# Optimization experiments

Hardware: AMD Instinct MI355X
Metric: run time of the kernel (lower is better)

The kernel has to match this reference:

```python
import jax, jax.numpy as jnp
import numpy as np

B, N, D, E, R, K = 4, 2048, 1024, 8, 256, 2


def setup_inputs() -> dict:
    key = jax.random.key(0)
    ks = jax.random.split(key, 5)
    scale = 0.02
    return {
        "x": jax.random.normal(ks[0], (B, N, D), dtype=jnp.float32),
        "gate_w": jax.random.normal(ks[1], (D, E), dtype=jnp.float32) * scale,
        "Wu": jax.random.normal(ks[2], (E, D, R), dtype=jnp.float32) * scale,
        "Wv": jax.random.normal(ks[3], (E, D, R), dtype=jnp.float32) * scale,
        "Wo": jax.random.normal(ks[4], (E, R, D), dtype=jnp.float32) * scale,
    }


def reference(x, gate_w, Wu, Wv, Wo):
    # Router: top-k over expert logits, softmax over the selected k logits.
    logits = jnp.einsum("bnd,de->bne", x, gate_w)          # [B,N,E]
    topv, topi = jax.lax.top_k(logits, K)                    # [B,N,K]
    w = jax.nn.softmax(topv, axis=-1)                        # [B,N,K]

    # Dense all-expert SwiGLU (matches reference semantics: every expert
    # computed for every token, then gathered by top-k index).
    u = jnp.einsum("bnd,edr->bner", x, Wu)                  # [B,N,E,R]
    v = jnp.einsum("bnd,edr->bner", x, Wv)                  # [B,N,E,R]
    s = jax.nn.silu(u) * v                                   # [B,N,E,R]
    Y = jnp.einsum("bner,erd->bned", s, Wo)                 # [B,N,E,D]

    # Gather the k selected experts per token and combine with gate weights.
    y_sel = jnp.take_along_axis(Y, topi[..., None], axis=2)  # [B,N,K,D]
    out = jnp.einsum("bnkd,bnk->bnd", y_sel, w)             # [B,N,D]
    return out
```

## Files before the change

### kernel.cpp

```cpp
#include <hip/hip_runtime.h>
#include <math.h>

#define BN 8192
#define DIM 1024
#define NE 8
#define RR 256

using bf16x8 = __attribute__((ext_vector_type(8))) short;
using f32x4  = __attribute__((ext_vector_type(4))) float;

__device__ inline unsigned short f2bf(float f) {
    unsigned int u = __float_as_uint(f);
    u = (u + 0x7fffu + ((u >> 16) & 1u)) >> 16;
    return (unsigned short)u;
}

__global__ __launch_bounds__(256) void k_gwt(const float* __restrict__ gw,
                                             float* __restrict__ gwT) {
    int i = blockIdx.x * 256 + threadIdx.x;
    float v = gw[i];
    int d = i >> 3, e = i & 7;
    gwT[e * DIM + d] = v;
}

__global__ __launch_bounds__(256) void k_router3(const float* __restrict__ x,
                                                 const float* __restrict__ gwT,
                                                 int* __restrict__ topi,
                                                 float* __restrict__ topw,
                                                 unsigned short* __restrict__ xb) {
    int wid  = (blockIdx.x * blockDim.x + threadIdx.x) >> 6;
    int lane = threadIdx.x & 63;
    const float* xp = x + (size_t)wid * DIM + lane * 4;
    unsigned short* xbp = xb + (size_t)wid * DIM + lane * 4;
    float4 acc[NE];
#pragma unroll
    for (int e = 0; e < NE; ++e) acc[e] = float4{0.f, 0.f, 0.f, 0.f};
#pragma unroll
    for (int k = 0; k < 4; ++k) {
        float4 xv = *(const float4*)(xp + k * 256);
        ushort4 us = { f2bf(xv.x), f2bf(xv.y), f2bf(xv.z), f2bf(xv.w) };
        *(ushort4*)(xbp + k * 256) = us;
#pragma unroll
        for (int e = 0; e < NE; ++e) {
            float4 gv = *(const float4*)(gwT + e * DIM + k * 256 + lane * 4);
            acc[e].x += xv.x * gv.x; acc[e].y += xv.y * gv.y;
            acc[e].z += xv.z * gv.z; acc[e].w += xv.w * gv.w;
        }
    }
    float lg[NE];
#pragma unroll
    for (int e = 0; e < NE; ++e)
        lg[e] = (acc[e].x + acc[e].y) + (acc[e].z + acc[e].w);
#pragma unroll
    for (int off = 32; off; off >>= 1) {
#pragma unroll
        for (int e = 0; e < NE; ++e) lg[e] += __shfl_xor(lg[e], off, 64);
    }
    if (lane == 0) {
        float best = lg[0]; int bi = 0;
#pragma unroll
        for (int e = 1; e < NE; ++e) if (lg[e] > best) { best = lg[e]; bi = e; }
        float sec = -3.4e38f; int si = 0;
#pragma unroll
        for (int e = 0; e < NE; ++e) if (e != bi && lg[e] > sec) { sec = lg[e]; si = e; }
        float p  = __expf(sec - best);
        float w0 = 1.f / (1.f + p);
        float w1 = p * w0;
        topi[wid * 2 + 0] = bi;  topw[wid * 2 + 0] = w0;
        topi[wid * 2 + 1] = si;  topw[wid * 2 + 1] = w1;
    }
}

__global__ __launch_bounds__(1024) void k_count_scan(const int* __restrict__ topi,
                                                     int* __restrict__ counts,
                                                     int* __restrict__ offsets,
                                                     int* __restrict__ fill,
                                                     int* __restrict__ tileOff) {
    __shared__ int sh[1024 * NE];
    int tid = threadIdx.x;
    int c[NE];
#pragma unroll
    for (int j = 0; j < NE; ++j) c[j] = 0;
    const int4* tp = (const int4*)topi;
    for (int i = tid; i < BN * 2 / 4; i += 1024) {
        int4 v = tp[i];
#pragma unroll
        for (int j = 0; j < NE; ++j)
            c[j] += (v.x == j) + (v.y == j) + (v.z == j) + (v.w == j);
    }
#pragma unroll
    for (int j = 0; j < NE; ++j) sh[tid * NE + j] = c[j];
    __syncthreads();
    for (int s = 512; s > 0; s >>= 1) {
        if (tid < s) {
#pragma unroll
            for (int j = 0; j < NE; ++j) sh[tid * NE + j] += sh[(tid + s) * NE + j];
        }
        __syncthreads();
    }
    if (tid == 0) {
        int acc = 0, tacc = 0;
        for (int j = 0; j < NE; ++j) {
            int cj = sh[j];
            counts[j]  = cj;
            offsets[j] = acc;   acc  += cj;
            tileOff[j] = tacc;  tacc += (cj + 63) >> 6;
        }
        tileOff[NE] = tacc;
    }
    if (tid < NE) fill[tid] = 0;
}

__global__ __launch_bounds__(256) void k_fill2(const int* __restrict__ topi,
                                               const float* __restrict__ topw,
                                               const int* __restrict__ offsets,
                                               int* __restrict__ fill,
                                               int* __restrict__ btok,
                                               float* __restrict__ bw,
                                               int* __restrict__ slotOf) {
    int tid = threadIdx.x;
    int i = blockIdx.x * 256 + tid;
    int w = tid >> 6, lane = tid & 63;
    int e = topi[i];
    float wt = topw[i];

    __shared__ int waveCnt[4][NE];
    __shared__ int wavePre[4][NE];
    __shared__ int baseSh[NE];

    int myrank = 0;
    unsigned long long lt = (1ull << lane) - 1ull;
#pragma unroll
    for (int j = 0; j < NE; ++j) {
        unsigned long long m = __ballot(e == j);
        if (e == j) myrank = __popcll(m & lt);
        if (lane == 0) waveCnt[w][j] = __popcll(m);
    }
    __syncthreads();
    if (tid < NE) {
        int j = tid, acc = 0;
#pragma unroll
        for (int ww = 0; ww < 4; ++ww) { wavePre[ww][j] = acc; acc += waveCnt[ww][j]; }
        baseSh[j] = atomicAdd(&fill[j], acc);
    }
    __syncthreads();
    int slot = offsets[e] + baseSh[e] + wavePre[w][e] + myrank;
    btok[slot] = i >> 1;
    bw[slot]   = wt;
    slotOf[i]  = slot;
}

__global__ __launch_bounds__(256) void k_cvt3(const float* __restrict__ Wu,
                                              const float* __restrict__ Wv,
                                              const float* __restrict__ Wo,
                                              unsigned short* __restrict__ Wub,
                                              unsigned short* __restrict__ Wvb,
                                              unsigned short* __restrict__ Wob) {
    int z = blockIdx.y;
    int which = z >> 3, e = z & 7;
    int tile = blockIdx.x;
    const float* in; unsigned short* out;
    int M, N, n0, m0;
    if (which < 2) {
        M = DIM; N = RR;
        n0 = (tile & 7) * 32;  m0 = (tile >> 3) * 32;
        in = which ? Wv : Wu;  out = which ? Wvb : Wub;
    } else {
        M = RR; N = DIM;
        n0 = (tile & 31) * 32; m0 = (tile >> 5) * 32;
        in = Wo; out = Wob;
    }
    __shared__ float t[32][33];
    int tx = threadIdx.x & 31, ty = threadIdx.x >> 5;
    const float* inE = in + (size_t)e * M * N;
    unsigned short* outE = out + (size_t)e * M * N;
#pragma unroll
    for (int i = ty; i < 32; i += 8)
        t[i][tx] = inE[(size_t)(m0 + i) * N + n0 + tx];
    __syncthreads();
#pragma unroll
    for (int i = ty; i < 32; i += 8)
        outE[(size_t)(n0 + i) * M + m0 + tx] = f2bf(t[tx][i]);
}

__global__ __launch_bounds__(256, 2) void k_uv(
        const unsigned short* __restrict__ xb,
        const unsigned short* __restrict__ Wub,
        const unsigned short* __restrict__ Wvb,
        const int* __restrict__ counts,
        const int* __restrict__ offsets,
        const int* __restrict__ tileOff,
        const int* __restrict__ btok,
        const float* __restrict__ bw,
        unsigned short* __restrict__ Sbuf) {
    int rt = blockIdx.x & 3;
    int mt_lin = blockIdx.x >> 2;
    if (mt_lin >= tileOff[NE]) return;
    int e = 0;
#pragma unroll
    for (int j = 1; j < NE; ++j) if (mt_lin >= tileOff[j]) e = j;
    int t0 = (mt_lin - tileOff[e]) * 64;
    int ne = counts[e];
    int nt = min(64, ne - t0);
    int start = offsets[e] + t0;

    int tid = threadIdx.x;
    int w = tid >> 6, lane = tid & 63;
    int m16 = lane & 15, quad = lane >> 4;
    int wm = w & 1, wn = w >> 1;

    __shared__ unsigned short As[64][72];
    __shared__ unsigned short Bs[128][72];
    __shared__ int   tokL[64];
    __shared__ float gwL[64];

    if (tid < 64) {
        tokL[tid] = (tid < nt) ? btok[start + tid] : btok[start];
        gwL[tid]  = (tid < nt) ? bw[start + tid] : 0.f;
    }
    __syncthreads();

    const unsigned short* WuE = Wub + (size_t)e * RR * DIM + (size_t)rt * 64 * DIM;
    const unsigned short* WvE = Wvb + (size_t)e * RR * DIM + (size_t)rt * 64 * DIM;

    int arow = tid >> 2, apart = tid & 3;
    const unsigned short* asrc = xb + (size_t)tokL[arow] * DIM + apart * 16;
    int brow = tid >> 1, bhalf = tid & 1;
    const unsigned short* bsrc =
        (brow < 64 ? WuE + (size_t)brow * DIM : WvE + (size_t)(brow - 64) * DIM)
        + bhalf * 32;

    f32x4 accU[2][2], accV[2][2];
    f32x4 zz = {0.f, 0.f, 0.f, 0.f};
#pragma unroll
    for (int mt = 0; mt < 2; ++mt)
#pragma unroll
        for (int nl = 0; nl < 2; ++nl) { accU[mt][nl] = zz; accV[mt][nl] = zz; }

    uint4 pa0 = *(const uint4*)(asrc);
    uint4 pa1 = *(const uint4*)(asrc + 8);
    uint4 pb0 = *(const uint4*)(bsrc);
    uint4 pb1 = *(const uint4*)(bsrc + 8);
    uint4 pb2 = *(const uint4*)(bsrc + 16);
    uint4 pb3 = *(const uint4*)(bsrc + 24);

    for (int kt = 0; kt < 16; ++kt) {
        __syncthreads();
        *(uint4*)&As[arow][apart * 16]      = pa0;
        *(uint4*)&As[arow][apart * 16 + 8]  = pa1;
        *(uint4*)&Bs[brow][bhalf * 32]      = pb0;
        *(uint4*)&Bs[brow][bhalf * 32 + 8]  = pb1;
        *(uint4*)&Bs[brow][bhalf * 32 + 16] = pb2;
        *(uint4*)&Bs[brow][bhalf * 32 + 24] = pb3;
        __syncthreads();
        if (kt < 15) {
            int k1 = (kt + 1) * 64;
            pa0 = *(const uint4*)(asrc + k1);
            pa1 = *(const uint4*)(asrc + k1 + 8);
            pb0 = *(const uint4*)(bsrc + k1);
            pb1 = *(const uint4*)(bsrc + k1 + 8);
            pb2 = *(const uint4*)(bsrc + k1 + 16);
            pb3 = *(const uint4*)(bsrc + k1 + 24);
        }
#pragma unroll
        for (int ks = 0; ks < 2; ++ks) {
            bf16x8 a[2], bu[2], bv[2];
#pragma unroll
            for (int mt = 0; mt < 2; ++mt)
                a[mt] = *(const bf16x8*)&As[wm * 32 + mt * 16 + m16][ks * 32 + quad * 8];
#pragma unroll
            for (int nl = 0; nl < 2; ++nl) {
                bu[nl] = *(const bf16x8*)&Bs[wn * 32 + nl * 16 + m16][ks * 32 + quad * 8];
                bv[nl] = *(const bf16x8*)&Bs[64 + wn * 32 + nl * 16 + m16][ks * 32 + quad * 8];
            }
#pragma unroll
            for (int nl = 0; nl < 2; ++nl)
#pragma unroll
                for (int mt = 0; mt < 2; ++mt) {
                    accU[mt][nl] = __builtin_amdgcn_mfma_f32_16x16x32_bf16(a[mt], bu[nl], accU[mt][nl], 0, 0, 0);
                    accV[mt][nl] = __builtin_amdgcn_mfma_f32_16x16x32_bf16(a[mt], bv[nl], accV[mt][nl], 0, 0, 0);
                }
        }
    }

#pragma unroll
    for (int mt = 0; mt < 2; ++mt)
#pragma unroll
        for (int nl = 0; nl < 2; ++nl)
#pragma unroll
            for (int reg = 0; reg < 4; ++reg) {
                int trow = wm * 32 + mt * 16 + quad * 4 + reg;
                int rcol = rt * 64 + wn * 32 + nl * 16 + m16;
                float u = accU[mt][nl][reg], v = accV[mt][nl][reg];
                float s = (u / (1.f + __expf(-u))) * v * gwL[trow];
                if (trow < nt)
                    Sbuf[(size_t)(start + trow) * RR + rcol] = f2bf(s);
            }
}

__global__ __launch_bounds__(256, 2) void k_down(
        const unsigned short* __restrict__ Sbuf,
        const unsigned short* __restrict__ Wob,
        const int* __restrict__ counts,
        const int* __restrict__ offsets,
        const int* __restrict__ tileOff,
        const int* __restrict__ btok,
        float* __restrict__ ybuf,
        float* __restrict__ out) {
    int nd = blockIdx.x & 7;
    int mt_lin = blockIdx.x >> 3;
    if (mt_lin >= tileOff[NE]) return;
    int e = 0;
#pragma unroll
    for (int j = 1; j < NE; ++j) if (mt_lin >= tileOff[j]) e = j;
    int t0 = (mt_lin - tileOff[e]) * 64;
    int ne = counts[e];
    int nt = min(64, ne - t0);
    int start = offsets[e] + t0;

    int tid = threadIdx.x;
    int w = tid >> 6, lane = tid & 63;
    int m16 = lane & 15, quad = lane >> 4;
    int wm = w & 1, wn = w >> 1;

    __shared__ unsigned short As[64][72];
    __shared__ unsigned short Bs[128][72];
    __shared__ int tokL[64];

    if (tid < 64)
        tokL[tid] = (tid < nt) ? btok[start + tid] : btok[start];
    __syncthreads();

    const unsigned short* WoE = Wob + (size_t)e * DIM * RR + (size_t)nd * 128 * RR;

    int arow = tid >> 2, apart = tid & 3;
    const unsigned short* asrc = Sbuf + (size_t)(start + arow) * RR + apart * 16;
    int brow = tid >> 1, bhalf = tid & 1;
    const unsigned short* bsrc = WoE + (size_t)brow * RR + bhalf * 32;

    f32x4 acc[2][4];
    f32x4 zz = {0.f, 0.f, 0.f, 0.f};
#pragma unroll
    for (int mt = 0; mt < 2; ++mt)
#pragma unroll
        for (int nl = 0; nl < 4; ++nl) acc[mt][nl] = zz;

    uint4 pa0 = *(const uint4*)(asrc);
    uint4 pa1 = *(const uint4*)(asrc + 8);
    uint4 pb0 = *(const uint4*)(bsrc);
    uint4 pb1 = *(const uint4*)(bsrc + 8);
    uint4 pb2 = *(const uint4*)(bsrc + 16);
    uint4 pb3 = *(const uint4*)(bsrc + 24);

    for (int kt = 0; kt < 4; ++kt) {
        __syncthreads();
        *(uint4*)&As[arow][apart * 16]      = pa0;
        *(uint4*)&As[arow][apart * 16 + 8]  = pa1;
        *(uint4*)&Bs[brow][bhalf * 32]      = pb0;
        *(uint4*)&Bs[brow][bhalf * 32 + 8]  = pb1;
        *(uint4*)&Bs[brow][bhalf * 32 + 16] = pb2;
        *(uint4*)&Bs[brow][bhalf * 32 + 24] = pb3;
        __syncthreads();
        if (kt < 3) {
            int k1 = (kt + 1) * 64;
            pa0 = *(const uint4*)(asrc + k1);
            pa1 = *(const uint4*)(asrc + k1 + 8);
            pb0 = *(const uint4*)(bsrc + k1);
            pb1 = *(const uint4*)(bsrc + k1 + 8);
            pb2 = *(const uint4*)(bsrc + k1 + 16);
            pb3 = *(const uint4*)(bsrc + k1 + 24);
        }
#pragma unroll
        for (int ks = 0; ks < 2; ++ks) {
            bf16x8 a[2], b[4];
#pragma unroll
            for (int mt = 0; mt < 2; ++mt)
                a[mt] = *(const bf16x8*)&As[wm * 32 + mt * 16 + m16][ks * 32 + quad * 8];
#pragma unroll
            for (int nl = 0; nl < 4; ++nl)
                b[nl] = *(const bf16x8*)&Bs[wn * 64 + nl * 16 + m16][ks * 32 + quad * 8];
#pragma unroll
            for (int nl = 0; nl < 4; ++nl)
#pragma unroll
                for (int mt = 0; mt < 2; ++mt)
                    acc[mt][nl] = __builtin_amdgcn_mfma_f32_16x16x32_bf16(a[mt], b[nl], acc[mt][nl], 0, 0, 0);
        }
    }

    if (ybuf) {
#pragma unroll
        for (int mt = 0; mt < 2; ++mt)
#pragma unroll
            for (int nl = 0; nl < 4; ++nl)
#pragma unroll
                for (int reg = 0; reg < 4; ++reg) {
                    int srow = wm * 32 + mt * 16 + quad * 4 + reg;
                    int d    = nd * 128 + wn * 64 + nl * 16 + m16;
                    if (srow < nt)
                        ybuf[(size_t)(start + srow) * DIM + d] = acc[mt][nl][reg];
                }
    } else {
#pragma unroll
        for (int mt = 0; mt < 2; ++mt)
#pragma unroll
            for (int nl = 0; nl < 4; ++nl)
#pragma unroll
                for (int reg = 0; reg < 4; ++reg) {
                    int srow = wm * 32 + mt * 16 + quad * 4 + reg;
                    int d    = nd * 128 + wn * 64 + nl * 16 + m16;
                    if (srow < nt)
                        atomicAdd(&out[(size_t)tokL[srow] * DIM + d], acc[mt][nl][reg]);
                }
    }
}

__global__ __launch_bounds__(256) void k_combine(const float* __restrict__ ybuf,
                                                 const int* __restrict__ slotOf,
                                                 float* __restrict__ out) {
    int t   = blockIdx.x;
    int seg = threadIdx.x;
    int s0 = slotOf[t * 2 + 0];
    int s1 = slotOf[t * 2 + 1];
    float4 a = *(const float4*)(ybuf + (size_t)s0 * DIM + seg * 4);
    float4 b = *(const float4*)(ybuf + (size_t)s1 * DIM + seg * 4);
    float4 r = { a.x + b.x, a.y + b.y, a.z + b.z, a.w + b.w };
    *(float4*)(out + (size_t)t * DIM + seg * 4) = r;
}

extern "C" void kernel_launch(void* const* d_in, const int* in_sizes, int n_in,
                              void* d_out, int out_size, void* d_ws, size_t ws_size,
                              hipStream_t stream) {
    const float* x  = (const float*)d_in[0];
    const float* gw = (const float*)d_in[1];
    const float* Wu = (const float*)d_in[2];
    const float* Wv = (const float*)d_in[3];
    const float* Wo = (const float*)d_in[4];
    float* out = (float*)d_out;

    int*   wsi     = (int*)d_ws;
    int*   counts  = wsi + 0;
    int*   offsets = wsi + 8;
    int*   fill    = wsi + 16;
    int*   tileOff = wsi + 24;
    int*   topi    = wsi + 48;
    float* topw    = (float*)(wsi + 48 + 16384);
    int*   btok    = wsi + 48 + 32768;
    float* bw      = (float*)(wsi + 48 + 49152);
    int*   slotOf  = wsi + 48 + 65536;
    float* gwT     = (float*)((char*)d_ws + 327872);

    const size_t off_xb  = 393216;
    const size_t off_wub = off_xb  + (size_t)BN * DIM * 2;
    const size_t off_wvb = off_wub + (size_t)NE * RR * DIM * 2;
    const size_t off_wob = off_wvb + (size_t)NE * RR * DIM * 2;
    const size_t off_sb  = off_wob + (size_t)NE * DIM * RR * 2;
    const size_t off_yb  = off_sb  + (size_t)(BN * 2 + 128) * RR * 2;
    const size_t need_yb = off_yb  + (size_t)BN * 2 * DIM * 4;

    unsigned short* xb   = (unsigned short*)((char*)d_ws + off_xb);
    unsigned short* Wub  = (unsigned short*)((char*)d_ws + off_wub);
    unsigned short* Wvb  = (unsigned short*)((char*)d_ws + off_wvb);
    unsigned short* Wob  = (unsigned short*)((char*)d_ws + off_wob);
    unsigned short* Sbuf = (unsigned short*)((char*)d_ws + off_sb);
    bool use_ybuf = (ws_size >= need_yb);
    float* ybuf = use_ybuf ? (float*)((char*)d_ws + off_yb) : nullptr;

    k_gwt<<<dim3(DIM * NE / 256), 256, 0, stream>>>(gw, gwT);
    k_router3<<<dim3(BN / 4), 256, 0, stream>>>(x, gwT, topi, topw, xb);
    k_count_scan<<<1, 1024, 0, stream>>>(topi, counts, offsets, fill, tileOff);
    k_fill2<<<dim3(BN * 2 / 256), 256, 0, stream>>>(topi, topw, offsets, fill,
                                                    btok, bw, slotOf);
    k_cvt3<<<dim3(256, 24), 256, 0, stream>>>(Wu, Wv, Wo, Wub, Wvb, Wob);

    if (!use_ybuf)
        hipMemsetAsync(d_out, 0, (size_t)BN * DIM * sizeof(float), stream);

    k_uv<<<dim3(264 * 4), 256, 0, stream>>>(xb, Wub, Wvb, counts, offsets, tileOff,
                                            btok, bw, Sbuf);
    k_down<<<dim3(264 * 8), 256, 0, stream>>>(Sbuf, Wob, counts, offsets, tileOff,
                                              btok, ybuf, out);
    if (use_ybuf)
        k_combine<<<dim3(BN), 256, 0, stream>>>(ybuf, slotOf, out);
}
```

Before: 204.8 us.

## Load expert weights directly into registers and widen per-block tiles in MoE GEMMs

In both the up/gate and down-projection kernels, the B-operand (weights) is now read straight from global memory into MFMA register fragments with a one-step register prefetch, instead of being staged through shared memory. Each wave now covers a full 64-row by 64-column slice, so k_uv covers all 256 R columns per block and k_down covers 256 output columns per block, cutting grid sizes by 4x and 2x. The A tile is double-buffered in LDS, which drops one barrier per k-step. The cost is much higher register pressure from the 32 accumulators in k_uv, which may lower occupancy, and fewer blocks in k_uv (264), which may underfill the GPU.

```diff
diff --git a/kernel.cpp b/kernel.cpp
--- a/kernel.cpp
+++ b/kernel.cpp
@@ -193,8 +193,7 @@
         const int* __restrict__ btok,
         const float* __restrict__ bw,
         unsigned short* __restrict__ Sbuf) {
-    int rt = blockIdx.x & 3;
-    int mt_lin = blockIdx.x >> 2;
+    int mt_lin = blockIdx.x;
     if (mt_lin >= tileOff[NE]) return;
     int e = 0;
 #pragma unroll
@@ -207,10 +206,8 @@
     int tid = threadIdx.x;
     int w = tid >> 6, lane = tid & 63;
     int m16 = lane & 15, quad = lane >> 4;
-    int wm = w & 1, wn = w >> 1;
-
-    __shared__ unsigned short As[64][72];
-    __shared__ unsigned short Bs[128][72];
+
+    __shared__ unsigned short As[2][64][72];
     __shared__ int   tokL[64];
     __shared__ float gwL[64];
 
@@ -220,77 +217,78 @@
     }
     __syncthreads();
 
-    const unsigned short* WuE = Wub + (size_t)e * RR * DIM + (size_t)rt * 64 * DIM;
-    const unsigned short* WvE = Wvb + (size_t)e * RR * DIM + (size_t)rt * 64 * DIM;
+    const unsigned short* WuE = Wub + (size_t)e * RR * DIM;
+    const unsigned short* WvE = Wvb + (size_t)e * RR * DIM;
 
     int arow = tid >> 2, apart = tid & 3;
     const unsigned short* asrc = xb + (size_t)tokL[arow] * DIM + apart * 16;
-    int brow = tid >> 1, bhalf = tid & 1;
-    const unsigned short* bsrc =
-        (brow < 64 ? WuE + (size_t)brow * DIM : WvE + (size_t)(brow - 64) * DIM)
-        + bhalf * 32;
-
-    f32x4 accU[2][2], accV[2][2];
+
+    const unsigned short* buBase = WuE + (size_t)(w * 64 + m16) * DIM + quad * 8;
+    const unsigned short* bvBase = WvE + (size_t)(w * 64 + m16) * DIM + quad * 8;
+
+    f32x4 accU[4][4], accV[4][4];
     f32x4 zz = {0.f, 0.f, 0.f, 0.f};
 #pragma unroll
-    for (int mt = 0; mt < 2; ++mt)
-#pragma unroll
-        for (int nl = 0; nl < 2; ++nl) { accU[mt][nl] = zz; accV[mt][nl] = zz; }
+    for (int mt = 0; mt < 4; ++mt)
+#pragma unroll
+        for (int nl = 0; nl < 4; ++nl) { accU[mt][nl] = zz; accV[mt][nl] = zz; }
 
     uint4 pa0 = *(const uint4*)(asrc);
     uint4 pa1 = *(const uint4*)(asrc + 8);
-    uint4 pb0 = *(const uint4*)(bsrc);
-    uint4 pb1 = *(const uint4*)(bsrc + 8);
-    uint4 pb2 = *(const uint4*)(bsrc + 16);
-    uint4 pb3 = *(const uint4*)(bsrc + 24);
+    uint4 bu[4], bv[4];
+#pragma unroll
+    for (int nl = 0; nl < 4; ++nl) {
+        bu[nl] = *(const uint4*)(buBase + nl * 16 * DIM);
+        bv[nl] = *(const uint4*)(bvBase + nl * 16 * DIM);
+    }
 
     for (int kt = 0; kt < 16; ++kt) {
+        int buf = kt & 1;
+        *(uint4*)&As[buf][arow][apart * 16]     = pa0;
+        *(uint4*)&As[buf][arow][apart * 16 + 8] = pa1;
+        if (kt < 15) {
+            pa0 = *(const uint4*)(asrc + (kt + 1) * 64);
+            pa1 = *(const uint4*)(asrc + (kt + 1) * 64 + 8);
+        }
         __syncthreads();
-        *(uint4*)&As[arow][apart * 16]      = pa0;
-        *(uint4*)&As[arow][apart * 16 + 8]  = pa1;
-        *(uint4*)&Bs[brow][bhalf * 32]      = pb0;
-        *(uint4*)&Bs[brow][bhalf * 32 + 8]  = pb1;
-        *(uint4*)&Bs[brow][bhalf * 32 + 16] = pb2;
-        *(uint4*)&Bs[brow][bhalf * 32 + 24] = pb3;
-        __syncthreads();
-        if (kt < 15) {
-            int k1 = (kt + 1) * 64;
-            pa0 = *(const uint4*)(asrc + k1);
-            pa1 = *(const uint4*)(asrc + k1 + 8);
-            pb0 = *(const uint4*)(bsrc + k1);
-            pb1 = *(const uint4*)(bsrc + k1 + 8);
-            pb2 = *(const uint4*)(bsrc + k1 + 16);
-            pb3 = *(const uint4*)(bsrc + k1 + 24);
-        }
 #pragma unroll
         for (int ks = 0; ks < 2; ++ks) {
-            bf16x8 a[2], bu[2], bv[2];
-#pragma unroll
-            for (int mt = 0; mt < 2; ++mt)
-                a[mt] = *(const bf16x8*)&As[wm * 32 + mt * 16 + m16][ks * 32 + quad * 8];
-#pragma unroll
-            for (int nl = 0; nl < 2; ++nl) {
-                bu[nl] = *(const bf16x8*)&Bs[wn * 32 + nl * 16 + m16][ks * 32 + quad * 8];
-                bv[nl] = *(const bf16x8*)&Bs[64 + wn * 32 + nl * 16 + m16][ks * 32 + quad * 8];
+            uint4 nu[4], nv[4];
+            int kn = kt * 64 + ks * 32 + 32;
+            if (kt < 15 || ks < 1) {
+#pragma unroll
+                for (int nl = 0; nl < 4; ++nl) {
+                    nu[nl] = *(const uint4*)(buBase + nl * 16 * DIM + kn);
+                    nv[nl] = *(const uint4*)(bvBase + nl * 16 * DIM + kn);
+                }
             }
-#pragma unroll
-            for (int nl = 0; nl < 2; ++nl)
-#pragma unroll
-                for (int mt = 0; mt < 2; ++mt) {
-                    accU[mt][nl] = __builtin_amdgcn_mfma_f32_16x16x32_bf16(a[mt], bu[nl], accU[mt][nl], 0, 0, 0);
-                    accV[mt][nl] = __builtin_amdgcn_mfma_f32_16x16x32_bf16(a[mt], bv[nl], accV[mt][nl], 0, 0, 0);
+            bf16x8 a[4];
+#pragma unroll
+            for (int mt = 0; mt < 4; ++mt)
+                a[mt] = *(const bf16x8*)&As[buf][mt * 16 + m16][ks * 32 + quad * 8];
+#pragma unroll
+            for (int nl = 0; nl < 4; ++nl) {
+                bf16x8 fu = __builtin_bit_cast(bf16x8, bu[nl]);
+                bf16x8 fv = __builtin_bit_cast(bf16x8, bv[nl]);
+#pragma unroll
+                for (int mt = 0; mt < 4; ++mt) {
+                    accU[mt][nl] = __builtin_amdgcn_mfma_f32_16x16x32_bf16(a[mt], fu, accU[mt][nl], 0, 0, 0);
+                    accV[mt][nl] = __builtin_amdgcn_mfma_f32_16x16x32_bf16(a[mt], fv, accV[mt][nl], 0, 0, 0);
                 }
-        }
-    }
-
-#pragma unroll
-    for (int mt = 0; mt < 2; ++mt)
-#pragma unroll
-        for (int nl = 0; nl < 2; ++nl)
+            }
+#pragma unroll
+            for (int nl = 0; nl < 4; ++nl) { bu[nl] = nu[nl]; bv[nl] = nv[nl]; }
+        }
+    }
+
+#pragma unroll
+    for (int mt = 0; mt < 4; ++mt)
+#pragma unroll
+        for (int nl = 0; nl < 4; ++nl)
 #pragma unroll
             for (int reg = 0; reg < 4; ++reg) {
-                int trow = wm * 32 + mt * 16 + quad * 4 + reg;
-                int rcol = rt * 64 + wn * 32 + nl * 16 + m16;
+                int trow = mt * 16 + quad * 4 + reg;
+                int rcol = w * 64 + nl * 16 + m16;
                 float u = accU[mt][nl][reg], v = accV[mt][nl][reg];
                 float s = (u / (1.f + __expf(-u))) * v * gwL[trow];
                 if (trow < nt)
@@ -307,8 +305,8 @@
         const int* __restrict__ btok,
         float* __restrict__ ybuf,
         float* __restrict__ out) {
-    int nd = blockIdx.x & 7;
-    int mt_lin = blockIdx.x >> 3;
+    int nd = blockIdx.x & 3;
+    int mt_lin = blockIdx.x >> 2;
     if (mt_lin >= tileOff[NE]) return;
     int e = 0;
 #pragma unroll
@@ -321,93 +319,90 @@
     int tid = threadIdx.x;
     int w = tid >> 6, lane = tid & 63;
     int m16 = lane & 15, quad = lane >> 4;
-    int wm = w & 1, wn = w >> 1;
-
-    __shared__ unsigned short As[64][72];
-    __shared__ unsigned short Bs[128][72];
+
+    __shared__ unsigned short As[2][64][72];
     __shared__ int tokL[64];
 
     if (tid < 64)
         tokL[tid] = (tid < nt) ? btok[start + tid] : btok[start];
     __syncthreads();
 
-    const unsigned short* WoE = Wob + (size_t)e * DIM * RR + (size_t)nd * 128 * RR;
+    const unsigned short* WoE = Wob + (size_t)e * DIM * RR;
 
     int arow = tid >> 2, apart = tid & 3;
     const unsigned short* asrc = Sbuf + (size_t)(start + arow) * RR + apart * 16;
-    int brow = tid >> 1, bhalf = tid & 1;
-    const unsigned short* bsrc = WoE + (size_t)brow * RR + bhalf * 32;
-
-    f32x4 acc[2][4];
+
+    const unsigned short* bBase = WoE + (size_t)(nd * 256 + w * 64 + m16) * RR + quad * 8;
+
+    f32x4 acc[4][4];
     f32x4 zz = {0.f, 0.f, 0.f, 0.f};
 #pragma unroll
-    for (int mt = 0; mt < 2; ++mt)
+    for (int mt = 0; mt < 4; ++mt)
 #pragma unroll
         for (int nl = 0; nl < 4; ++nl) acc[mt][nl] = zz;
 
     uint4 pa0 = *(const uint4*)(asrc);
     uint4 pa1 = *(const uint4*)(asrc + 8);
-    uint4 pb0 = *(const uint4*)(bsrc);
-    uint4 pb1 = *(const uint4*)(bsrc + 8);
-    uint4 pb2 = *(const uint4*)(bsrc + 16);
-    uint4 pb3 = *(const uint4*)(bsrc + 24);
+    uint4 b[4];
+#pragma unroll
+    for (int nl = 0; nl < 4; ++nl)
+        b[nl] = *(const uint4*)(bBase + nl * 16 * RR);
 
     for (int kt = 0; kt < 4; ++kt) {
+        int buf = kt & 1;
+        *(uint4*)&As[buf][arow][apart * 16]     = pa0;
+        *(uint4*)&As[buf][arow][apart * 16 + 8] = pa1;
+        if (kt < 3) {
+            pa0 = *(const uint4*)(asrc + (kt + 1) * 64);
+            pa1 = *(const uint4*)(asrc + (kt + 1) * 64 + 8);
+        }
         __syncthreads();
-        *(uint4*)&As[arow][apart * 16]      = pa0;
-        *(uint4*)&As[arow][apart * 16 + 8]  = pa1;
-        *(uint4*)&Bs[brow][bhalf * 32]      = pb0;
-        *(uint4*)&Bs[brow][bhalf * 32 + 8]  = pb1;
-        *(uint4*)&Bs[brow][bhalf * 32 + 16] = pb2;
-        *(uint4*)&Bs[brow][bhalf * 32 + 24] = pb3;
-        __syncthreads();
-        if (kt < 3) {
-            int k1 = (kt + 1) * 64;
-            pa0 = *(const uint4*)(asrc + k1);
-            pa1 = *(const uint4*)(asrc + k1 + 8);
-            pb0 = *(const uint4*)(bsrc + k1);
-            pb1 = *(const uint4*)(bsrc + k1 + 8);
-            pb2 = *(const uint4*)(bsrc + k1 + 16);
-            pb3 = *(const uint4*)(bsrc + k1 + 24);
-        }
 #pragma unroll
         for (int ks = 0; ks < 2; ++ks) {
-            bf16x8 a[2], b[4];
-#pragma unroll
-            for (int mt = 0; mt < 2; ++mt)
-                a[mt] = *(const bf16x8*)&As[wm * 32 + mt * 16 + m16][ks * 32 + quad * 8];
+            uint4 nb[4];
+            int kn = kt * 64 + ks * 32 + 32;
+            if (kt < 3 || ks < 1) {
+#pragma unroll
+                for (int nl = 0; nl < 4; ++nl)
+                    nb[nl] = *(const uint4*)(bBase + nl * 16 * RR + kn);
+            }
+            bf16x8 a[4];
+#pragma unroll
+            for (int mt = 0; mt < 4; ++mt)
+                a[mt] = *(const bf16x8*)&As[buf][mt * 16 + m16][ks * 32 + quad * 8];
+#pragma unroll
+            for (int nl = 0; nl < 4; ++nl) {
+                bf16x8 fb = __builtin_bit_cast(bf16x8, b[nl]);
+#pragma unroll
+                for (int mt = 0; mt < 4; ++mt)
+                    acc[mt][nl] = __builtin_amdgcn_mfma_f32_16x16x32_bf16(a[mt], fb, acc[mt][nl], 0, 0, 0);
+            }
+#pragma unroll
+            for (int nl = 0; nl < 4; ++nl) b[nl] = nb[nl];
+        }
+    }
+
+    if (ybuf) {
+#pragma unroll
+        for (int mt = 0; mt < 4; ++mt)
 #pragma unroll
             for (int nl = 0; nl < 4; ++nl)
-                b[nl] = *(const bf16x8*)&Bs[wn * 64 + nl * 16 + m16][ks * 32 + quad * 8];
-#pragma unroll
-            for (int nl = 0; nl < 4; ++nl)
-#pragma unroll
-                for (int mt = 0; mt < 2; ++mt)
-                    acc[mt][nl] = __builtin_amdgcn_mfma_f32_16x16x32_bf16(a[mt], b[nl], acc[mt][nl], 0, 0, 0);
-        }
-    }
-
-    if (ybuf) {
-#pragma unroll
-        for (int mt = 0; mt < 2; ++mt)
-#pragma unroll
-            for (int nl = 0; nl < 4; ++nl)
 #pragma unroll
                 for (int reg = 0; reg < 4; ++reg) {
-                    int srow = wm * 32 + mt * 16 + quad * 4 + reg;
-                    int d    = nd * 128 + wn * 64 + nl * 16 + m16;
+                    int srow = mt * 16 + quad * 4 + reg;
+                    int d    = nd * 256 + w * 64 + nl * 16 + m16;
                     if (srow < nt)
                         ybuf[(size_t)(start + srow) * DIM + d] = acc[mt][nl][reg];
                 }
     } else {
 #pragma unroll
-        for (int mt = 0; mt < 2; ++mt)
+        for (int mt = 0; mt < 4; ++mt)
 #pragma unroll
             for (int nl = 0; nl < 4; ++nl)
 #pragma unroll
                 for (int reg = 0; reg < 4; ++reg) {
-                    int srow = wm * 32 + mt * 16 + quad * 4 + reg;
-                    int d    = nd * 128 + wn * 64 + nl * 16 + m16;
+                    int srow = mt * 16 + quad * 4 + reg;
+                    int d    = nd * 256 + w * 64 + nl * 16 + m16;
                     if (srow < nt)
                         atomicAdd(&out[(size_t)tokL[srow] * DIM + d], acc[mt][nl][reg]);
                 }
@@ -475,9 +470,9 @@
     if (!use_ybuf)
         hipMemsetAsync(d_out, 0, (size_t)BN * DIM * sizeof(float), stream);
 
-    k_uv<<<dim3(264 * 4), 256, 0, stream>>>(xb, Wub, Wvb, counts, offsets, tileOff,
-                                            btok, bw, Sbuf);
-    k_down<<<dim3(264 * 8), 256, 0, stream>>>(Sbuf, Wob, counts, offsets, tileOff,
+    k_uv<<<dim3(264), 256, 0, stream>>>(xb, Wub, Wvb, counts, offsets, tileOff,
+                                        btok, bw, Sbuf);
+    k_down<<<dim3(264 * 4), 256, 0, stream>>>(Sbuf, Wob, counts, offsets, tileOff,
                                               btok, ybuf, out);
     if (use_ybuf)
         k_combine<<<dim3(BN), 256, 0, stream>>>(ybuf, slotOf, out);
```

After: 243.7 us. +19.0%, slower.
